# Kernel optimization log

Measured on AMD Instinct MI355X. Metric: run time of the kernel, lower is better.

Reference implementation:

```python
import jax, jax.numpy as jnp
import numpy as np

EPS = 1e-12  # F.normalize eps
REGION = (5, 5)
STRIDE = (2, 2)


def _l2norm(v, axis):
    n = jnp.sqrt(jnp.sum(v * v, axis=axis, keepdims=True))
    return v / jnp.maximum(n, EPS)


def setup_inputs() -> dict:
    key = jax.random.key(0)
    k1, k2, k3 = jax.random.split(key, 3)
    N, C, H, W, K = 4, 128, 40, 40, 64
    x = jax.random.normal(k1, (N, C, H, W), dtype=jnp.float32)
    conv_w = jax.random.normal(k2, (K, C), dtype=jnp.float32)  # 1x1 conv, no bias (vladv2=False)
    centroids = jax.random.uniform(k3, (K, C), dtype=jnp.float32)  # torch.rand init
    return {"x": x, "conv_w": conv_w, "centroids": centroids}


def reference(x, conv_w, centroids):
    N, C, H, W = x.shape
    K = centroids.shape[0]
    # descriptor-wise L2 normalization over channels
    x = _l2norm(x, axis=1)
    # 1x1 conv -> soft assignment over clusters
    soft_assign = jnp.einsum('nchw,kc->nkhw', x, conv_w)
    soft_assign = jax.nn.softmax(soft_assign, axis=1)
    # soft-assign-weighted residuals: [N, K, C, H, W]
    resid = x[:, None, :, :, :] - centroids[None, :, :, None, None]
    store = resid * soft_assign[:, :, None, :, :]
    # global VLAD (sum over all spatial locations)
    vlad_full = store.sum(axis=(-1, -2))  # [N, K, C]
    # regional average pooling (kernel 5x5, stride 2, valid)
    Hout = (H - REGION[0]) // STRIDE[0] + 1
    Wout = (W - REGION[1]) // STRIDE[1] + 1
    pooled = jax.lax.reduce_window(
        store.reshape(N, K * C, H, W), 0.0, jax.lax.add,
        (1, 1, REGION[0], REGION[1]), (1, 1, STRIDE[0], STRIDE[1]), 'VALID')
    pooled = pooled / (REGION[0] * REGION[1])
    # regional VLAD: intra-norm over C, flatten, global L2 norm
    vlad = pooled.reshape(N, K, C, Hout, Wout)
    vlad = _l2norm(vlad, axis=2)
    vlad = vlad.reshape(N, K * C, Hout * Wout)
    vlad = _l2norm(vlad, axis=1)
    # full VLAD: intra-norm over C, flatten, global L2 norm
    vlad_full = _l2norm(vlad_full, axis=2)
    vlad_full = vlad_full.reshape(N, K * C)
    vlad_full = _l2norm(vlad_full, axis=1)
    return vlad, vlad_full
```

## Files before the change

kernel.cpp:

```cpp
#include <hip/hip_runtime.h>

#define EPSN 1e-12f

#define NB   4
#define CC   128
#define KK_  64
#define HH   40
#define WW   40
#define HWP  1600
#define HO   18
#define WO   18
#define HWO  324
#define KCC  8192

#define WS_T   0
#define WS_XN  10616832
#define WS_A   11436032
#define WS_GP  11845632
#define WS_G0  12369920

static __device__ __forceinline__ int swzk1(int c, int px){ return c ^ ((px & 31) << 2); }

__device__ __forceinline__ void gl_lds16(const float* g, float* l)
{
  __builtin_amdgcn_global_load_lds(
      (const __attribute__((address_space(1))) void*)g,
      (__attribute__((address_space(3))) void*)l, 16, 0, 0);
}

__global__ __launch_bounds__(1024) void k1_norm_assign(
    const float* __restrict__ x, const float* __restrict__ w,
    float* __restrict__ xn, float* __restrict__ aout)
{
  __shared__ __align__(16) float xs[64][128];
  __shared__ float ds[64][65];
  __shared__ float invs[64];
  const int t = threadIdx.x;
  const int b = blockIdx.x;
  const int n = b / 25;
  const int pixb = (b % 25) * 64;
  const float* xb = x + (size_t)n * CC * HWP + pixb;

  {
    const int px = t & 63, cs = t >> 6;
    #pragma unroll
    for (int j = 0; j < 8; ++j) {
      const int c = cs + 16 * j;
      xs[px][swzk1(c, px)] = xb[c * HWP + px];
    }
  }
  __syncthreads();
  {
    const int p = t >> 4, q = t & 15;
    float ss = 0.f;
    #pragma unroll
    for (int j = 0; j < 8; ++j) {
      const float v = xs[p][swzk1(q + 16 * j, p)];
      ss += v * v;
    }
    ss += __shfl_xor(ss, 1); ss += __shfl_xor(ss, 2);
    ss += __shfl_xor(ss, 4); ss += __shfl_xor(ss, 8);
    if (q == 0) invs[p] = 1.f / fmaxf(sqrtf(ss), EPSN);
  }
  __syncthreads();
  {
    float* xno = xn + ((size_t)n * HWP + pixb) * CC;
    #pragma unroll
    for (int rr = 0; rr < 8; ++rr) {
      const int i = t + rr * 1024;
      const int pp = i >> 7, c = i & 127;
      const float v = xs[pp][swzk1(c, pp)] * invs[pp];
      xs[pp][swzk1(c, pp)] = v;
      xno[i] = v;
    }
  }
  __syncthreads();
  {
    const int lane = t & 63;
    const int wv = __builtin_amdgcn_readfirstlane(t >> 6);
    float acc[4] = {0.f, 0.f, 0.f, 0.f};
    #pragma unroll 4
    for (int c4 = 0; c4 < 32; ++c4) {
      const float4 x4 = *(const float4*)&xs[lane][(c4 << 2) ^ ((lane & 31) << 2)];
      #pragma unroll
      for (int kk = 0; kk < 4; ++kk) {
        const float* wr = &w[(wv * 4 + kk) * CC + (c4 << 2)];
        acc[kk] += x4.x * wr[0] + x4.y * wr[1] + x4.z * wr[2] + x4.w * wr[3];
      }
    }
    #pragma unroll
    for (int kk = 0; kk < 4; ++kk) ds[lane][wv * 4 + kk] = acc[kk];
  }
  __syncthreads();
  {
    const int p = t >> 4, q = t & 15;
    float v[4]; float m = -3.4e38f;
    #pragma unroll
    for (int kk = 0; kk < 4; ++kk){ v[kk] = ds[p][q + 16 * kk]; m = fmaxf(m, v[kk]); }
    m = fmaxf(m, __shfl_xor(m, 1)); m = fmaxf(m, __shfl_xor(m, 2));
    m = fmaxf(m, __shfl_xor(m, 4)); m = fmaxf(m, __shfl_xor(m, 8));
    float s = 0.f;
    #pragma unroll
    for (int kk = 0; kk < 4; ++kk){ v[kk] = __expf(v[kk] - m); s += v[kk]; }
    s += __shfl_xor(s, 1); s += __shfl_xor(s, 2);
    s += __shfl_xor(s, 4); s += __shfl_xor(s, 8);
    const float is = 1.f / s;
    #pragma unroll
    for (int kk = 0; kk < 4; ++kk) ds[p][q + 16 * kk] = v[kk] * is;
  }
  __syncthreads();
  {
    float* ao = aout + ((size_t)n * HWP + pixb) * KK_;
    #pragma unroll
    for (int rr = 0; rr < 4; ++rr) {
      const int i = t + rr * 1024;
      ao[i] = ds[i >> 6][i & 63];
    }
  }
}

__device__ __forceinline__ void dots25(const float (*a_s)[64], const float (*xs)[128],
                                       int k0, int c0, float acc[16], float s0[4])
{
  #pragma unroll 5
  for (int p = 0; p < 25; ++p) {
    const float4 a4 = *(const float4*)&a_s[p][k0];
    const float4 x4 = *(const float4*)&xs[p][c0];
    const float av[4] = {a4.x, a4.y, a4.z, a4.w};
    #pragma unroll
    for (int m = 0; m < 4; ++m) {
      s0[m] += av[m];
      acc[m * 4 + 0] += av[m] * x4.x;
      acc[m * 4 + 1] += av[m] * x4.y;
      acc[m * 4 + 2] += av[m] * x4.z;
      acc[m * 4 + 3] += av[m] * x4.w;
    }
  }
}

__global__ __launch_bounds__(512, 4) void k2_main(
    const float* __restrict__ xn, const float* __restrict__ aw,
    const float* __restrict__ cent, float* __restrict__ T,
    float* __restrict__ Gpart, float* __restrict__ G0part)
{
  __shared__ __align__(16) float a_s[28][64];
  __shared__ __align__(16) float xs[26][128];
  __shared__ float red[8];
  const int t = threadIdx.x;
  const int lane = t & 63;
  const int wv = t >> 6;
  const int h = lane >> 5;
  const int l5 = lane & 31;
  const int c0 = l5 << 2;
  const int k0 = wv * 8 + h * 4;
  const int bid = (blockIdx.x & 7) * 170 + (blockIdx.x >> 3);

  float acc[16];
  #pragma unroll
  for (int j = 0; j < 16; ++j) acc[j] = 0.f;
  float s0[4];
  #pragma unroll
  for (int m = 0; m < 4; ++m) s0[m] = 0.f;

  if (bid < 1296) {
    const int n = bid / HWO, r = bid % HWO, ho = r / WO, wo = r % WO;
    if (wv < 7) {
      const int row = 4 * wv + (lane >> 4);
      const int pix = (2 * ho + row / 5) * WW + 2 * wo + row % 5;
      gl_lds16(aw + ((size_t)n * HWP + pix) * KK_ + ((lane & 15) << 2),
               &a_s[4 * wv][0]);
    }
    {
      const int row = 2 * wv + (lane >> 5);
      const int pix = (2 * ho + row / 5) * WW + 2 * wo + row % 5;
      gl_lds16(xn + ((size_t)n * HWP + pix) * CC + ((lane & 31) << 2),
               &xs[2 * wv][0]);
    }
    if (wv < 5) {
      const int j = wv + 8;
      const int row = 2 * j + (lane >> 5);
      const int pix = (2 * ho + row / 5) * WW + 2 * wo + row % 5;
      gl_lds16(xn + ((size_t)n * HWP + pix) * CC + ((lane & 31) << 2),
               &xs[2 * j][0]);
    }
    __syncthreads();

    dots25(a_s, xs, k0, c0, acc, s0);

    float ssm[4], rnm[4];
    #pragma unroll
    for (int m = 0; m < 4; ++m) {
      const int k = k0 + m;
      const float4 c4 = *(const float4*)&cent[(size_t)k * CC + c0];
      const float cv[4] = {c4.x, c4.y, c4.z, c4.w};
      float ss = 0.f;
      #pragma unroll
      for (int d = 0; d < 4; ++d) {
        const float pv = (acc[m * 4 + d] - cv[d] * s0[m]) * 0.04f;
        acc[m * 4 + d] = pv;
        ss += pv * pv;
      }
      ssm[m] = ss;
    }
    #pragma unroll
    for (int off = 1; off <= 16; off <<= 1) {
      #pragma unroll
      for (int m = 0; m < 4; ++m) ssm[m] += __shfl_xor(ssm[m], off);
    }
    float gpl = 0.f;
    #pragma unroll
    for (int m = 0; m < 4; ++m) {
      rnm[m] = 1.f / fmaxf(sqrtf(ssm[m]), EPSN);
      gpl += ssm[m] * rnm[m] * rnm[m];
    }
    gpl += __shfl_xor(gpl, 32);
    if (lane == 0) red[wv] = gpl;
    __syncthreads();
    float gtot = 0.f;
    #pragma unroll
    for (int i = 0; i < 8; ++i) gtot += red[i];
    const float gi = 1.f / fmaxf(sqrtf(gtot), EPSN);

    float* tb = T + ((size_t)n * HWO + r) * KCC;
    #pragma unroll
    for (int m = 0; m < 4; ++m) {
      const float sc = rnm[m] * gi;
      float4 v;
      v.x = acc[m * 4 + 0] * sc; v.y = acc[m * 4 + 1] * sc;
      v.z = acc[m * 4 + 2] * sc; v.w = acc[m * 4 + 3] * sc;
      *(float4*)&tb[(size_t)(k0 + m) * CC + c0] = v;
    }
  } else {
    const int pid = bid - 1296;
    const int n = pid >> 4, ch = pid & 15;
    #pragma unroll 1
    for (int rr = 0; rr < 4; ++rr) {
      const int pb = n * HWP + ch * 100 + rr * 25;
      if (wv < 7) {
        const int row = 4 * wv + (lane >> 4);
        gl_lds16(aw + (size_t)(pb + row) * KK_ + ((lane & 15) << 2),
                 &a_s[4 * wv][0]);
      }
      {
        const int row = 2 * wv + (lane >> 5);
        gl_lds16(xn + (size_t)(pb + row) * CC + ((lane & 31) << 2),
                 &xs[2 * wv][0]);
      }
      if (wv < 5) {
        const int j = wv + 8;
        const int row = 2 * j + (lane >> 5);
        gl_lds16(xn + (size_t)(pb + row) * CC + ((lane & 31) << 2),
                 &xs[2 * j][0]);
      }
      __syncthreads();
      dots25(a_s, xs, k0, c0, acc, s0);
      __syncthreads();
    }
    if (l5 == 0) {
      #pragma unroll
      for (int m = 0; m < 4; ++m)
        G0part[(size_t)pid * KK_ + k0 + m] = s0[m];
    }
    float* gb = Gpart + (size_t)pid * KCC;
    #pragma unroll
    for (int m = 0; m < 4; ++m) {
      float4 v;
      v.x = acc[m * 4 + 0]; v.y = acc[m * 4 + 1];
      v.z = acc[m * 4 + 2]; v.w = acc[m * 4 + 3];
      *(float4*)&gb[(size_t)(k0 + m) * CC + c0] = v;
    }
  }
}

__global__ __launch_bounds__(256) void k4_transpose(
    const float* __restrict__ T, float* __restrict__ out)
{
  __shared__ float tile[112][65];
  const int t = threadIdx.x;
  const int b = blockIdx.x;
  const int n = b / 384;
  const int rem = b % 384;
  const int kcT = rem / 3, rT = rem % 3;
  const int kc0 = kcT * 64;
  const int r0 = rT * 112;
  const int rows = (rT == 2) ? 100 : 112;
  const int w = t >> 6, lane = t & 63;

  for (int rr = w; rr < rows; rr += 4)
    tile[rr][lane] = T[((size_t)n * HWO + r0 + rr) * KCC + kc0 + lane];
  __syncthreads();

  #pragma unroll
  for (int j = 0; j < 16; ++j) {
    const int kcl = w + 4 * j;
    float* orow = out + (size_t)n * KCC * HWO + (size_t)(kc0 + kcl) * HWO + r0;
    orow[lane] = tile[lane][kcl];
    if (lane + 64 < rows) orow[64 + lane] = tile[64 + lane][kcl];
  }
}

__global__ __launch_bounds__(1024) void k3_full(
    const float* __restrict__ Gpart, const float* __restrict__ G0part,
    const float* __restrict__ cent, float* __restrict__ outF)
{
  __shared__ float red[16];
  const int n = blockIdx.x;
  const int t = threadIdx.x;
  const int k = t >> 4, cg16 = t & 15;
  const int c0 = cg16 * 8;

  float acc[8];
  #pragma unroll
  for (int j = 0; j < 8; ++j) acc[j] = 0.f;
  float g0 = 0.f;
  #pragma unroll 1
  for (int ch = 0; ch < 16; ++ch) {
    const float* gp = Gpart + ((size_t)(n * 16 + ch)) * KCC + (size_t)k * CC + c0;
    const float4 a4 = *(const float4*)(gp);
    const float4 b4 = *(const float4*)(gp + 4);
    acc[0] += a4.x; acc[1] += a4.y; acc[2] += a4.z; acc[3] += a4.w;
    acc[4] += b4.x; acc[5] += b4.y; acc[6] += b4.z; acc[7] += b4.w;
    g0 += G0part[(size_t)(n * 16 + ch) * KK_ + k];
  }

  float ss = 0.f;
  #pragma unroll
  for (int j = 0; j < 8; ++j) {
    const float v = acc[j] - cent[(size_t)k * CC + c0 + j] * g0;
    acc[j] = v;
    ss += v * v;
  }
  ss += __shfl_xor(ss, 1); ss += __shfl_xor(ss, 2);
  ss += __shfl_xor(ss, 4); ss += __shfl_xor(ss, 8);
  const float rn = 1.f / fmaxf(sqrtf(ss), EPSN);
  float part = (cg16 == 0) ? ss * rn * rn : 0.f;
  #pragma unroll
  for (int o = 1; o < 64; o <<= 1) part += __shfl_xor(part, o);
  if ((t & 63) == 0) red[t >> 6] = part;
  __syncthreads();
  float tot = 0.f;
  #pragma unroll
  for (int i = 0; i < 16; ++i) tot += red[i];
  const float scale = rn * (1.f / fmaxf(sqrtf(tot), EPSN));
  #pragma unroll
  for (int j = 0; j < 8; ++j)
    outF[(size_t)n * KCC + (size_t)k * CC + c0 + j] = acc[j] * scale;
}

extern "C" void kernel_launch(void* const* d_in, const int* in_sizes, int n_in,
                              void* d_out, int out_size, void* d_ws, size_t ws_size,
                              hipStream_t stream)
{
  const float* x    = (const float*)d_in[0];
  const float* w    = (const float*)d_in[1];
  const float* cent = (const float*)d_in[2];
  float* out = (float*)d_out;
  float* ws  = (float*)d_ws;

  float* T  = ws + WS_T;
  float* xn = ws + WS_XN;
  float* aw = ws + WS_A;
  float* gp = ws + WS_GP;
  float* g0 = ws + WS_G0;

  k1_norm_assign<<<dim3(100), dim3(1024), 0, stream>>>(x, w, xn, aw);
  k2_main<<<dim3(1360), dim3(512), 0, stream>>>(xn, aw, cent, T, gp, g0);
  k4_transpose<<<dim3(1536), dim3(256), 0, stream>>>(T, out);
  k3_full<<<dim3(NB), dim3(1024), 0, stream>>>(gp, g0, cent,
                                               out + (size_t)NB * KCC * HWO);
}
```

Measured before the change: 128.8 us.

## Compute two adjacent pooling windows per block and fuse full-VLAD into transpose kernel

Each k2 block now computes two horizontally adjacent 5x5 regional windows at once, loading a 5x7 pixel patch and sharing the three overlapping columns. This reduces global-to-LDS traffic and halves the block count, at the cost of doubled accumulator registers. The full-VLAD reduction kernel is merged into the transpose kernel as four extra blocks, which removes one launch and lets that work overlap with the transpose.

Measured after the change: 131.0 us. No clear change (+1.6%).

```diff
diff --git a/kernel.cpp b/kernel.cpp
--- a/kernel.cpp
+++ b/kernel.cpp
@@ -119,232 +119,250 @@
   }
 }
 
-__device__ __forceinline__ void dots25(const float (*a_s)[64], const float (*xs)[128],
-                                       int k0, int c0, float acc[16], float s0[4])
-{
-  #pragma unroll 5
-  for (int p = 0; p < 25; ++p) {
-    const float4 a4 = *(const float4*)&a_s[p][k0];
-    const float4 x4 = *(const float4*)&xs[p][c0];
-    const float av[4] = {a4.x, a4.y, a4.z, a4.w};
-    #pragma unroll
-    for (int m = 0; m < 4; ++m) {
-      s0[m] += av[m];
-      acc[m * 4 + 0] += av[m] * x4.x;
-      acc[m * 4 + 1] += av[m] * x4.y;
-      acc[m * 4 + 2] += av[m] * x4.z;
-      acc[m * 4 + 3] += av[m] * x4.w;
-    }
-  }
-}
-
 __global__ __launch_bounds__(512, 4) void k2_main(
     const float* __restrict__ xn, const float* __restrict__ aw,
     const float* __restrict__ cent, float* __restrict__ T,
     float* __restrict__ Gpart, float* __restrict__ G0part)
 {
-  __shared__ __align__(16) float a_s[28][64];
-  __shared__ __align__(16) float xs[26][128];
-  __shared__ float red[8];
+  __shared__ __align__(16) float a_s[2560];
+  __shared__ __align__(16) float xs[5120];
+  __shared__ float red[16];
   const int t = threadIdx.x;
   const int lane = t & 63;
   const int wv = t >> 6;
   const int h = lane >> 5;
-  const int l5 = lane & 31;
-  const int c0 = l5 << 2;
+  const int c0 = (lane & 31) << 2;
   const int k0 = wv * 8 + h * 4;
-  const int bid = (blockIdx.x & 7) * 170 + (blockIdx.x >> 3);
-
-  float acc[16];
+  const int bid = (blockIdx.x & 7) * 89 + (blockIdx.x >> 3);
+
+  float accA[16], accB[16];
   #pragma unroll
-  for (int j = 0; j < 16; ++j) acc[j] = 0.f;
-  float s0[4];
-  #pragma unroll
-  for (int m = 0; m < 4; ++m) s0[m] = 0.f;
-
-  if (bid < 1296) {
-    const int n = bid / HWO, r = bid % HWO, ho = r / WO, wo = r % WO;
-    if (wv < 7) {
-      const int row = 4 * wv + (lane >> 4);
-      const int pix = (2 * ho + row / 5) * WW + 2 * wo + row % 5;
-      gl_lds16(aw + ((size_t)n * HWP + pix) * KK_ + ((lane & 15) << 2),
-               &a_s[4 * wv][0]);
-    }
-    {
-      const int row = 2 * wv + (lane >> 5);
-      const int pix = (2 * ho + row / 5) * WW + 2 * wo + row % 5;
-      gl_lds16(xn + ((size_t)n * HWP + pix) * CC + ((lane & 31) << 2),
-               &xs[2 * wv][0]);
-    }
-    if (wv < 5) {
-      const int j = wv + 8;
-      const int row = 2 * j + (lane >> 5);
-      const int pix = (2 * ho + row / 5) * WW + 2 * wo + row % 5;
-      gl_lds16(xn + ((size_t)n * HWP + pix) * CC + ((lane & 31) << 2),
-               &xs[2 * j][0]);
+  for (int j = 0; j < 16; ++j) { accA[j] = 0.f; accB[j] = 0.f; }
+  float s0A[4] = {0,0,0,0}, s0B[4] = {0,0,0,0};
+
+  if (bid < 648) {
+    const int n = bid / 162, rem = bid % 162;
+    const int ho = rem / 9, pr = rem % 9;
+    const int base = n * HWP + 2 * ho * WW + 4 * pr;
+    #pragma unroll
+    for (int i = 0; i < 4; ++i) {
+      const int id = wv + 8 * i;
+      if (id < 10) {
+        const int dy = id >> 1, cc = id & 1;
+        gl_lds16(aw + (size_t)(base + dy * WW) * KK_ + cc * 256 + ((lane) << 2),
+                 &a_s[dy * 512 + cc * 256]);
+      } else if (id < 30) {
+        const int rel = id - 10, dy = rel >> 2, cc = rel & 3;
+        gl_lds16(xn + (size_t)(base + dy * WW) * CC + cc * 256 + ((lane) << 2),
+                 &xs[dy * 1024 + cc * 256]);
+      }
     }
     __syncthreads();
 
-    dots25(a_s, xs, k0, c0, acc, s0);
-
-    float ssm[4], rnm[4];
+    for (int dy = 0; dy < 5; ++dy) {
+      #pragma unroll
+      for (int j = 0; j < 7; ++j) {
+        const float4 a4 = *(const float4*)&a_s[dy * 512 + j * 64 + k0];
+        const float4 x4 = *(const float4*)&xs[dy * 1024 + j * 128 + c0];
+        const float av[4] = {a4.x, a4.y, a4.z, a4.w};
+        if (j < 5) {
+          #pragma unroll
+          for (int m = 0; m < 4; ++m) {
+            s0A[m] += av[m];
+            accA[m*4+0] += av[m]*x4.x; accA[m*4+1] += av[m]*x4.y;
+            accA[m*4+2] += av[m]*x4.z; accA[m*4+3] += av[m]*x4.w;
+          }
+        }
+        if (j >= 2) {
+          #pragma unroll
+          for (int m = 0; m < 4; ++m) {
+            s0B[m] += av[m];
+            accB[m*4+0] += av[m]*x4.x; accB[m*4+1] += av[m]*x4.y;
+            accB[m*4+2] += av[m]*x4.z; accB[m*4+3] += av[m]*x4.w;
+          }
+        }
+      }
+    }
+
+    float ssmA[4], ssmB[4], rnmA[4], rnmB[4];
     #pragma unroll
     for (int m = 0; m < 4; ++m) {
-      const int k = k0 + m;
-      const float4 c4 = *(const float4*)&cent[(size_t)k * CC + c0];
+      const float4 c4 = *(const float4*)&cent[(size_t)(k0 + m) * CC + c0];
       const float cv[4] = {c4.x, c4.y, c4.z, c4.w};
-      float ss = 0.f;
+      float sa = 0.f, sb = 0.f;
       #pragma unroll
       for (int d = 0; d < 4; ++d) {
-        const float pv = (acc[m * 4 + d] - cv[d] * s0[m]) * 0.04f;
-        acc[m * 4 + d] = pv;
-        ss += pv * pv;
-      }
-      ssm[m] = ss;
+        const float pa = (accA[m*4+d] - cv[d] * s0A[m]) * 0.04f;
+        const float pb = (accB[m*4+d] - cv[d] * s0B[m]) * 0.04f;
+        accA[m*4+d] = pa; accB[m*4+d] = pb;
+        sa += pa * pa; sb += pb * pb;
+      }
+      ssmA[m] = sa; ssmB[m] = sb;
     }
     #pragma unroll
     for (int off = 1; off <= 16; off <<= 1) {
       #pragma unroll
-      for (int m = 0; m < 4; ++m) ssm[m] += __shfl_xor(ssm[m], off);
-    }
-    float gpl = 0.f;
+      for (int m = 0; m < 4; ++m) {
+        ssmA[m] += __shfl_xor(ssmA[m], off);
+        ssmB[m] += __shfl_xor(ssmB[m], off);
+      }
+    }
+    float gplA = 0.f, gplB = 0.f;
     #pragma unroll
     for (int m = 0; m < 4; ++m) {
-      rnm[m] = 1.f / fmaxf(sqrtf(ssm[m]), EPSN);
-      gpl += ssm[m] * rnm[m] * rnm[m];
-    }
-    gpl += __shfl_xor(gpl, 32);
-    if (lane == 0) red[wv] = gpl;
+      rnmA[m] = 1.f / fmaxf(sqrtf(ssmA[m]), EPSN);
+      rnmB[m] = 1.f / fmaxf(sqrtf(ssmB[m]), EPSN);
+      gplA += ssmA[m] * rnmA[m] * rnmA[m];
+      gplB += ssmB[m] * rnmB[m] * rnmB[m];
+    }
+    gplA += __shfl_xor(gplA, 32);
+    gplB += __shfl_xor(gplB, 32);
+    if (lane == 0) { red[wv] = gplA; red[8 + wv] = gplB; }
     __syncthreads();
-    float gtot = 0.f;
-    #pragma unroll
-    for (int i = 0; i < 8; ++i) gtot += red[i];
-    const float gi = 1.f / fmaxf(sqrtf(gtot), EPSN);
-
-    float* tb = T + ((size_t)n * HWO + r) * KCC;
+    float gtA = 0.f, gtB = 0.f;
+    #pragma unroll
+    for (int i = 0; i < 8; ++i) { gtA += red[i]; gtB += red[8 + i]; }
+    const float giA = 1.f / fmaxf(sqrtf(gtA), EPSN);
+    const float giB = 1.f / fmaxf(sqrtf(gtB), EPSN);
+
+    const int r0 = ho * 18 + 2 * pr;
+    float* tbA = T + ((size_t)n * HWO + r0) * KCC;
+    float* tbB = tbA + KCC;
     #pragma unroll
     for (int m = 0; m < 4; ++m) {
-      const float sc = rnm[m] * gi;
-      float4 v;
-      v.x = acc[m * 4 + 0] * sc; v.y = acc[m * 4 + 1] * sc;
-      v.z = acc[m * 4 + 2] * sc; v.w = acc[m * 4 + 3] * sc;
-      *(float4*)&tb[(size_t)(k0 + m) * CC + c0] = v;
+      const float sa = rnmA[m] * giA, sb = rnmB[m] * giB;
+      float4 va, vb;
+      va.x = accA[m*4+0]*sa; va.y = accA[m*4+1]*sa;
+      va.z = accA[m*4+2]*sa; va.w = accA[m*4+3]*sa;
+      vb.x = accB[m*4+0]*sb; vb.y = accB[m*4+1]*sb;
+      vb.z = accB[m*4+2]*sb; vb.w = accB[m*4+3]*sb;
+      *(float4*)&tbA[(size_t)(k0 + m) * CC + c0] = va;
+      *(float4*)&tbB[(size_t)(k0 + m) * CC + c0] = vb;
     }
   } else {
-    const int pid = bid - 1296;
+    const int pid = bid - 648;
     const int n = pid >> 4, ch = pid & 15;
     #pragma unroll 1
     for (int rr = 0; rr < 4; ++rr) {
       const int pb = n * HWP + ch * 100 + rr * 25;
-      if (wv < 7) {
-        const int row = 4 * wv + (lane >> 4);
-        gl_lds16(aw + (size_t)(pb + row) * KK_ + ((lane & 15) << 2),
-                 &a_s[4 * wv][0]);
-      }
-      {
-        const int row = 2 * wv + (lane >> 5);
-        gl_lds16(xn + (size_t)(pb + row) * CC + ((lane & 31) << 2),
-                 &xs[2 * wv][0]);
-      }
-      if (wv < 5) {
-        const int j = wv + 8;
-        const int row = 2 * j + (lane >> 5);
-        gl_lds16(xn + (size_t)(pb + row) * CC + ((lane & 31) << 2),
-                 &xs[2 * j][0]);
+      #pragma unroll
+      for (int i = 0; i < 3; ++i) {
+        const int id = wv + 8 * i;
+        if (id < 7) {
+          gl_lds16(aw + (size_t)pb * KK_ + id * 256 + (lane << 2),
+                   &a_s[id * 256]);
+        } else if (id < 20) {
+          const int rel = id - 7;
+          gl_lds16(xn + (size_t)pb * CC + rel * 256 + (lane << 2),
+                   &xs[rel * 256]);
+        }
       }
       __syncthreads();
-      dots25(a_s, xs, k0, c0, acc, s0);
+      #pragma unroll 5
+      for (int p = 0; p < 25; ++p) {
+        const float4 a4 = *(const float4*)&a_s[p * 64 + k0];
+        const float4 x4 = *(const float4*)&xs[p * 128 + c0];
+        const float av[4] = {a4.x, a4.y, a4.z, a4.w};
+        #pragma unroll
+        for (int m = 0; m < 4; ++m) {
+          s0A[m] += av[m];
+          accA[m*4+0] += av[m]*x4.x; accA[m*4+1] += av[m]*x4.y;
+          accA[m*4+2] += av[m]*x4.z; accA[m*4+3] += av[m]*x4.w;
+        }
+      }
       __syncthreads();
     }
-    if (l5 == 0) {
+    if ((lane & 31) == 0) {
       #pragma unroll
       for (int m = 0; m < 4; ++m)
-        G0part[(size_t)pid * KK_ + k0 + m] = s0[m];
+        G0part[(size_t)pid * KK_ + k0 + m] = s0A[m];
     }
     float* gb = Gpart + (size_t)pid * KCC;
     #pragma unroll
     for (int m = 0; m < 4; ++m) {
       float4 v;
-      v.x = acc[m * 4 + 0]; v.y = acc[m * 4 + 1];
-      v.z = acc[m * 4 + 2]; v.w = acc[m * 4 + 3];
+      v.x = accA[m*4+0]; v.y = accA[m*4+1];
+      v.z = accA[m*4+2]; v.w = accA[m*4+3];
       *(float4*)&gb[(size_t)(k0 + m) * CC + c0] = v;
     }
   }
 }
 
-__global__ __launch_bounds__(256) void k4_transpose(
-    const float* __restrict__ T, float* __restrict__ out)
+__global__ __launch_bounds__(256) void k4_trans_full(
+    const float* __restrict__ T, float* __restrict__ out,
+    const float* __restrict__ Gpart, const float* __restrict__ G0part,
+    const float* __restrict__ cent, float* __restrict__ outF)
 {
   __shared__ float tile[112][65];
+  __shared__ float red[4];
   const int t = threadIdx.x;
   const int b = blockIdx.x;
-  const int n = b / 384;
-  const int rem = b % 384;
-  const int kcT = rem / 3, rT = rem % 3;
-  const int kc0 = kcT * 64;
-  const int r0 = rT * 112;
-  const int rows = (rT == 2) ? 100 : 112;
-  const int w = t >> 6, lane = t & 63;
-
-  for (int rr = w; rr < rows; rr += 4)
-    tile[rr][lane] = T[((size_t)n * HWO + r0 + rr) * KCC + kc0 + lane];
-  __syncthreads();
-
-  #pragma unroll
-  for (int j = 0; j < 16; ++j) {
-    const int kcl = w + 4 * j;
-    float* orow = out + (size_t)n * KCC * HWO + (size_t)(kc0 + kcl) * HWO + r0;
-    orow[lane] = tile[lane][kcl];
-    if (lane + 64 < rows) orow[64 + lane] = tile[64 + lane][kcl];
-  }
-}
-
-__global__ __launch_bounds__(1024) void k3_full(
-    const float* __restrict__ Gpart, const float* __restrict__ G0part,
-    const float* __restrict__ cent, float* __restrict__ outF)
-{
-  __shared__ float red[16];
-  const int n = blockIdx.x;
-  const int t = threadIdx.x;
-  const int k = t >> 4, cg16 = t & 15;
-  const int c0 = cg16 * 8;
-
-  float acc[8];
-  #pragma unroll
-  for (int j = 0; j < 8; ++j) acc[j] = 0.f;
-  float g0 = 0.f;
-  #pragma unroll 1
-  for (int ch = 0; ch < 16; ++ch) {
-    const float* gp = Gpart + ((size_t)(n * 16 + ch)) * KCC + (size_t)k * CC + c0;
-    const float4 a4 = *(const float4*)(gp);
-    const float4 b4 = *(const float4*)(gp + 4);
-    acc[0] += a4.x; acc[1] += a4.y; acc[2] += a4.z; acc[3] += a4.w;
-    acc[4] += b4.x; acc[5] += b4.y; acc[6] += b4.z; acc[7] += b4.w;
-    g0 += G0part[(size_t)(n * 16 + ch) * KK_ + k];
-  }
-
-  float ss = 0.f;
-  #pragma unroll
-  for (int j = 0; j < 8; ++j) {
-    const float v = acc[j] - cent[(size_t)k * CC + c0 + j] * g0;
-    acc[j] = v;
-    ss += v * v;
-  }
-  ss += __shfl_xor(ss, 1); ss += __shfl_xor(ss, 2);
-  ss += __shfl_xor(ss, 4); ss += __shfl_xor(ss, 8);
-  const float rn = 1.f / fmaxf(sqrtf(ss), EPSN);
-  float part = (cg16 == 0) ? ss * rn * rn : 0.f;
-  #pragma unroll
-  for (int o = 1; o < 64; o <<= 1) part += __shfl_xor(part, o);
-  if ((t & 63) == 0) red[t >> 6] = part;
-  __syncthreads();
-  float tot = 0.f;
-  #pragma unroll
-  for (int i = 0; i < 16; ++i) tot += red[i];
-  const float scale = rn * (1.f / fmaxf(sqrtf(tot), EPSN));
-  #pragma unroll
-  for (int j = 0; j < 8; ++j)
-    outF[(size_t)n * KCC + (size_t)k * CC + c0 + j] = acc[j] * scale;
+
+  if (b < 1536) {
+    const int n = b / 384;
+    const int rem = b % 384;
+    const int kcT = rem / 3, rT = rem % 3;
+    const int kc0 = kcT * 64;
+    const int r0 = rT * 112;
+    const int rows = (rT == 2) ? 100 : 112;
+    const int w = t >> 6, lane = t & 63;
+
+    for (int rr = w; rr < rows; rr += 4)
+      tile[rr][lane] = T[((size_t)n * HWO + r0 + rr) * KCC + kc0 + lane];
+    __syncthreads();
+
+    #pragma unroll
+    for (int j = 0; j < 16; ++j) {
+      const int kcl = w + 4 * j;
+      float* orow = out + (size_t)n * KCC * HWO + (size_t)(kc0 + kcl) * HWO + r0;
+      orow[lane] = tile[lane][kcl];
+      if (lane + 64 < rows) orow[64 + lane] = tile[64 + lane][kcl];
+    }
+  } else {
+    const int n = b - 1536;
+    const int k = t >> 2, cg4 = t & 3;
+    const int c0 = cg4 * 32;
+
+    float acc[32];
+    #pragma unroll
+    for (int j = 0; j < 32; ++j) acc[j] = 0.f;
+    float g0 = 0.f;
+    #pragma unroll 1
+    for (int ch = 0; ch < 16; ++ch) {
+      const float* gp = Gpart + ((size_t)(n * 16 + ch)) * KCC + (size_t)k * CC + c0;
+      #pragma unroll
+      for (int j4 = 0; j4 < 8; ++j4) {
+        const float4 g4 = *(const float4*)(gp + (j4 << 2));
+        acc[j4*4+0] += g4.x; acc[j4*4+1] += g4.y;
+        acc[j4*4+2] += g4.z; acc[j4*4+3] += g4.w;
+      }
+      g0 += G0part[(size_t)(n * 16 + ch) * KK_ + k];
+    }
+
+    float ss = 0.f;
+    #pragma unroll
+    for (int j = 0; j < 32; ++j) {
+      const float v = acc[j] - cent[(size_t)k * CC + c0 + j] * g0;
+      acc[j] = v;
+      ss += v * v;
+    }
+    ss += __shfl_xor(ss, 1); ss += __shfl_xor(ss, 2);
+    const float rn = 1.f / fmaxf(sqrtf(ss), EPSN);
+    float part = (cg4 == 0) ? ss * rn * rn : 0.f;
+    #pragma unroll
+    for (int o = 1; o < 64; o <<= 1) part += __shfl_xor(part, o);
+    if ((t & 63) == 0) red[t >> 6] = part;
+    __syncthreads();
+    const float tot = red[0] + red[1] + red[2] + red[3];
+    const float scale = rn * (1.f / fmaxf(sqrtf(tot), EPSN));
+    #pragma unroll
+    for (int j4 = 0; j4 < 8; ++j4) {
+      float4 v;
+      v.x = acc[j4*4+0]*scale; v.y = acc[j4*4+1]*scale;
+      v.z = acc[j4*4+2]*scale; v.w = acc[j4*4+3]*scale;
+      *(float4*)&outF[(size_t)n * KCC + (size_t)k * CC + c0 + (j4 << 2)] = v;
+    }
+  }
 }
 
 extern "C" void kernel_launch(void* const* d_in, const int* in_sizes, int n_in,
@@ -364,8 +382,7 @@
   float* g0 = ws + WS_G0;
 
   k1_norm_assign<<<dim3(100), dim3(1024), 0, stream>>>(x, w, xn, aw);
-  k2_main<<<dim3(1360), dim3(512), 0, stream>>>(xn, aw, cent, T, gp, g0);
-  k4_transpose<<<dim3(1536), dim3(256), 0, stream>>>(T, out);
-  k3_full<<<dim3(NB), dim3(1024), 0, stream>>>(gp, g0, cent,
-                                               out + (size_t)NB * KCC * HWO);
-}
+  k2_main<<<dim3(712), dim3(512), 0, stream>>>(xn, aw, cent, T, gp, g0);
+  k4_trans_full<<<dim3(1540), dim3(256), 0, stream>>>(T, out, gp, g0, cent,
+                                                      out + (size_t)NB * KCC * HWO);
+}
```
